# Kernel optimization log

Measured on AMD Instinct MI355X. Metric: run time of the kernel, lower is better.

## Reference

```python
import jax, jax.numpy as jnp
import numpy as np

H = 1024
N_HEADS = 16
DK = H // N_HEADS
B = 4
S_TGT = 1024
S_SRC = 1024
LN_EPS = 1e-5


def _ln(x, g, b):
    m = jnp.mean(x, axis=-1, keepdims=True)
    v = jnp.mean(jnp.square(x - m), axis=-1, keepdims=True)
    return (x - m) * jax.lax.rsqrt(v + LN_EPS) * g + b


def _mha(q_in, k_in, v_in, wq, wk, wv, wo, mask):
    # Equivalent to torch split(hidden//n_splits)+cat(dim=0) head layout:
    # per-(batch,head) scaled dot-product attention.
    Bq, Sq, _ = q_in.shape
    Sk = k_in.shape[1]
    q = (q_in @ wq).reshape(Bq, Sq, N_HEADS, DK)
    k = (k_in @ wk).reshape(Bq, Sk, N_HEADS, DK)
    v = (v_in @ wv).reshape(Bq, Sk, N_HEADS, DK)
    scores = jnp.einsum('bqhd,bkhd->bhqk', q, k)
    if mask is not None:
        scores = jnp.where(mask[:, None, :, :], -jnp.inf, scores)
    attn = jax.nn.softmax(scores / np.sqrt(DK).astype(np.float32), axis=-1)
    ctx = jnp.einsum('bhqk,bkhd->bqhd', attn, v).reshape(Bq, Sq, H)
    return ctx @ wo


def setup_inputs() -> dict:
    key = jax.random.key(0)
    ks = jax.random.split(key, 16)
    std = 1.0 / np.sqrt(H)
    p = {
        'x': jax.random.normal(ks[0], (B, S_TGT, H), jnp.float32),
        'key_and_value': jax.random.normal(ks[1], (B, S_SRC, H), jnp.float32),
        'mask': jnp.zeros((B, S_TGT, S_SRC), jnp.bool_),  # no padding
        # causal mask: True above the diagonal (masked positions)
        'future_mask': jnp.broadcast_to(
            jnp.triu(jnp.ones((S_TGT, S_TGT), jnp.bool_), k=1), (B, S_TGT, S_TGT)),
        'sa_wq': jax.random.normal(ks[2], (H, H), jnp.float32) * std,
        'sa_wk': jax.random.normal(ks[3], (H, H), jnp.float32) * std,
        'sa_wv': jax.random.normal(ks[4], (H, H), jnp.float32) * std,
        'sa_wo': jax.random.normal(ks[5], (H, H), jnp.float32) * std,
        'ca_wq': jax.random.normal(ks[6], (H, H), jnp.float32) * std,
        'ca_wk': jax.random.normal(ks[7], (H, H), jnp.float32) * std,
        'ca_wv': jax.random.normal(ks[8], (H, H), jnp.float32) * std,
        'ca_wo': jax.random.normal(ks[9], (H, H), jnp.float32) * std,
        'fc_w1': jax.random.normal(ks[10], (H, 4 * H), jnp.float32) * std,
        'fc_b1': jnp.zeros((4 * H,), jnp.float32),
        'fc_w2': jax.random.normal(ks[11], (4 * H, H), jnp.float32) * (0.5 * std),
        'fc_b2': jnp.zeros((H,), jnp.float32),
        'ln1_g': jnp.ones((H,), jnp.float32), 'ln1_b': jnp.zeros((H,), jnp.float32),
        'ln2_g': jnp.ones((H,), jnp.float32), 'ln2_b': jnp.zeros((H,), jnp.float32),
        'ln3_g': jnp.ones((H,), jnp.float32), 'ln3_b': jnp.zeros((H,), jnp.float32),
    }
    return p


def reference(x, key_and_value, mask, future_mask,
              sa_wq, sa_wk, sa_wv, sa_wo,
              ca_wq, ca_wk, ca_wv, ca_wo,
              fc_w1, fc_b1, fc_w2, fc_b2,
              ln1_g, ln1_b, ln2_g, ln2_b, ln3_g, ln3_b):
    # prev is None path (training); dropout in eval mode = identity.
    z = _ln(x, ln1_g, ln1_b)
    z = x + _mha(z, z, z, sa_wq, sa_wk, sa_wv, sa_wo, future_mask)
    nkv = _ln(key_and_value, ln2_g, ln2_b)
    z = z + _mha(_ln(z, ln2_g, ln2_b), nkv, nkv, ca_wq, ca_wk, ca_wv, ca_wo, mask)
    h = jax.nn.relu(_ln(z, ln3_g, ln3_b) @ fc_w1 + fc_b1)
    z = z + (h @ fc_w2 + fc_b2)
    return z
```

## Files before the change

### kernel.cpp

```cpp
#include <hip/hip_runtime.h>
#include <hip/hip_bf16.h>

typedef __attribute__((ext_vector_type(8))) short short8;
typedef __attribute__((ext_vector_type(4))) float f32x4;
using bf16 = __hip_bfloat16;

__device__ __forceinline__ void gload16(const void* g, void* l) {
  __builtin_amdgcn_global_load_lds(
      (const __attribute__((address_space(1))) void*)g,
      (__attribute__((address_space(3))) void*)l, 16, 0, 0);
}

__device__ __forceinline__ short f2bf(float f) {
  bf16 h = __float2bfloat16(f);
  short s;
  __builtin_memcpy(&s, &h, 2);
  return s;
}

__device__ __forceinline__ float bf2f(unsigned short u) {
  unsigned int x = ((unsigned int)u) << 16;
  float f;
  __builtin_memcpy(&f, &x, 4);
  return f;
}

__global__ __launch_bounds__(256)
void wtr8(const float* w0, const float* w1, const float* w2, const float* w3,
          const float* w4, const float* w5, const float* w6, const float* w7,
          bf16* __restrict__ Wout) {
  __shared__ float tile[32][33];
  const float* w;
  switch (blockIdx.z) {
    case 0: w = w0; break; case 1: w = w1; break;
    case 2: w = w2; break; case 3: w = w3; break;
    case 4: w = w4; break; case 5: w = w5; break;
    case 6: w = w6; break; default: w = w7; break;
  }
  bf16* wt = Wout + (size_t)blockIdx.z * 1024 * 1024;
  const int tx = threadIdx.x & 31, ty = threadIdx.x >> 5;
  const int c0 = blockIdx.x * 32, r0 = blockIdx.y * 32;
#pragma unroll
  for (int i = 0; i < 4; ++i)
    tile[ty * 4 + i][tx] = w[(size_t)(r0 + ty * 4 + i) * 1024 + c0 + tx];
  __syncthreads();
#pragma unroll
  for (int i = 0; i < 4; ++i) {
    const int cc = ty * 4 + i;
    wt[(size_t)(c0 + cc) * 1024 + r0 + tx] = __float2bfloat16(tile[tx][cc]);
  }
}

__global__ __launch_bounds__(256)
void wtr(const float* __restrict__ w, bf16* __restrict__ wt, int R, int C) {
  __shared__ float tile[32][33];
  const int tx = threadIdx.x & 31, ty = threadIdx.x >> 5;
  const int c0 = blockIdx.x * 32, r0 = blockIdx.y * 32;
#pragma unroll
  for (int i = 0; i < 4; ++i)
    tile[ty * 4 + i][tx] = w[(size_t)(r0 + ty * 4 + i) * C + c0 + tx];
  __syncthreads();
#pragma unroll
  for (int i = 0; i < 4; ++i) {
    const int cc = ty * 4 + i;
    wt[(size_t)(c0 + cc) * R + r0 + tx] = __float2bfloat16(tile[tx][cc]);
  }
}

__global__ __launch_bounds__(256)
void ln_k(const float* __restrict__ x, const float* __restrict__ g,
          const float* __restrict__ b, bf16* __restrict__ y) {
  const int row = blockIdx.x, t = threadIdx.x;
  const int wv = t >> 6, l = t & 63;
  const float4 v = reinterpret_cast<const float4*>(x + (size_t)row * 1024)[t];
  float s = v.x + v.y + v.z + v.w;
  float s2 = v.x * v.x + v.y * v.y + v.z * v.z + v.w * v.w;
#pragma unroll
  for (int m = 1; m < 64; m <<= 1) {
    s += __shfl_xor(s, m, 64);
    s2 += __shfl_xor(s2, m, 64);
  }
  __shared__ float ps[4], ps2[4];
  if (l == 0) { ps[wv] = s; ps2[wv] = s2; }
  __syncthreads();
  s = ps[0] + ps[1] + ps[2] + ps[3];
  s2 = ps2[0] + ps2[1] + ps2[2] + ps2[3];
  const float mean = s * (1.f / 1024.f);
  const float var = s2 * (1.f / 1024.f) - mean * mean;
  const float rs = rsqrtf(var + 1e-5f);
  const float4 gg = reinterpret_cast<const float4*>(g)[t];
  const float4 bb = reinterpret_cast<const float4*>(b)[t];
  ushort4 o;
  o.x = (unsigned short)f2bf((v.x - mean) * rs * gg.x + bb.x);
  o.y = (unsigned short)f2bf((v.y - mean) * rs * gg.y + bb.y);
  o.z = (unsigned short)f2bf((v.z - mean) * rs * gg.z + bb.z);
  o.w = (unsigned short)f2bf((v.w - mean) * rs * gg.w + bb.w);
  reinterpret_cast<ushort4*>(y + (size_t)row * 1024)[t] = o;
}

__global__ __launch_bounds__(256)
void ffn_add4b(const ushort4* __restrict__ p0, const ushort4* __restrict__ p1,
               const ushort4* __restrict__ p2, const ushort4* __restrict__ p3,
               const float4* __restrict__ res, const float4* __restrict__ bias,
               float4* __restrict__ out) {
  const size_t i = (size_t)blockIdx.x * 256 + threadIdx.x;
  const ushort4 a = p0[i], b = p1[i], c = p2[i], d = p3[i];
  const float4 r = res[i];
  const float4 g = bias[i & 255];
  float4 o;
  o.x = (bf2f(a.x) + bf2f(b.x)) + (bf2f(c.x) + bf2f(d.x)) + r.x + g.x;
  o.y = (bf2f(a.y) + bf2f(b.y)) + (bf2f(c.y) + bf2f(d.y)) + r.y + g.y;
  o.z = (bf2f(a.z) + bf2f(b.z)) + (bf2f(c.z) + bf2f(d.z)) + r.z + g.z;
  o.w = (bf2f(a.w) + bf2f(b.w)) + (bf2f(c.w) + bf2f(d.w)) + r.w + g.w;
  out[i] = o;
}

template <int BM, int EPI>
__global__ __launch_bounds__(256, 2)
void gemm_bt(const bf16* __restrict__ A, const bf16* __restrict__ BT,
             const float* bias, const float* res, void* outp,
             int M, int N, int K, bf16* vtp, int nv0) {
  constexpr int WM = BM / 32;
  constexpr int APASS = BM / 32;
  __shared__ alignas(16) short al[2][BM * 64];
  __shared__ alignas(16) short bl[2][128 * 64];
  const int t = threadIdx.x;
  const int gx = N >> 7;
  const int nwg = gridDim.x * gridDim.y;
  int id = blockIdx.y * gridDim.x + blockIdx.x;
  id = (id & 7) * (nwg >> 3) + (id >> 3);
  const int bx = id % gx, by = id / gx;
  const int m0 = by * BM, n0 = bx * 128;
  const int wv = t >> 6, l = t & 63, lr = l & 15, lk = l >> 4;
  const int wr = wv >> 1, wc = wv & 1;
  const int tr = t >> 3, tc = (t & 7) * 8;
  const int tcs = (((t & 7) ^ (tr & 7)) * 8);
  const int cro0 = ((lk ^ (lr & 7)) * 8);
  const int cro1 = (((4 + lk) ^ (lr & 7)) * 8);

  f32x4 acc[WM][4];
#pragma unroll
  for (int i = 0; i < WM; ++i)
#pragma unroll
    for (int j = 0; j < 4; ++j) acc[i][j] = (f32x4)0.f;

#define STAGE(buf, k0)                                                        \
  do {                                                                        \
    _Pragma("unroll") for (int it = 0; it < APASS; ++it) {                    \
      const int row = it * 32 + tr;                                           \
      gload16(A + (size_t)(m0 + row) * K + (k0) + tcs,                        \
              (char*)&al[buf][row * 64 + tc]);                                \
    }                                                                         \
    _Pragma("unroll") for (int it = 0; it < 4; ++it) {                        \
      const int row = it * 32 + tr;                                           \
      gload16(BT + (size_t)(n0 + row) * K + (k0) + tcs,                       \
              (char*)&bl[buf][row * 64 + tc]);                                \
    }                                                                         \
  } while (0)

#define COMPUTE(cur)                                                          \
  do {                                                                        \
    _Pragma("unroll") for (int ks = 0; ks < 2; ++ks) {                        \
      const int cro = ks ? cro1 : cro0;                                       \
      short8 af[WM], bfv[4];                                                  \
      _Pragma("unroll") for (int m = 0; m < WM; ++m) af[m] =                  \
          *reinterpret_cast<const short8*>(                                   \
              &al[cur][(wr * (BM / 2) + m * 16 + lr) * 64 + cro]);            \
      _Pragma("unroll") for (int n = 0; n < 4; ++n) bfv[n] =                  \
          *reinterpret_cast<const short8*>(                                   \
              &bl[cur][(wc * 64 + n * 16 + lr) * 64 + cro]);                  \
      _Pragma("unroll") for (int m = 0; m < WM; ++m)                          \
          _Pragma("unroll") for (int n = 0; n < 4; ++n) acc[m][n] =           \
              __builtin_amdgcn_mfma_f32_16x16x32_bf16(af[m], bfv[n],          \
                                                      acc[m][n], 0, 0, 0);    \
    }                                                                         \
  } while (0)

  const int nt = K >> 6;
  if constexpr (BM == 64) {
    STAGE(0, 0);
    STAGE(1, 64);
    for (int tk = 0; tk < nt; ++tk) {
      const int cur = tk & 1;
      if (tk < nt - 1)
        asm volatile("s_waitcnt vmcnt(6)" ::: "memory");
      else
        asm volatile("s_waitcnt vmcnt(0)" ::: "memory");
      __builtin_amdgcn_s_barrier();
      COMPUTE(cur);
      if (tk + 2 < nt) {
        asm volatile("s_waitcnt lgkmcnt(0)" ::: "memory");
        __builtin_amdgcn_s_barrier();
        STAGE(cur, (tk + 2) << 6);
      }
    }
  } else {
    STAGE(0, 0);
    asm volatile("s_waitcnt vmcnt(0)" ::: "memory");
    __syncthreads();
    for (int tk = 0; tk < nt; ++tk) {
      const int cur = tk & 1;
      if (tk + 1 < nt) STAGE(cur ^ 1, (tk + 1) << 6);
      COMPUTE(cur);
      asm volatile("s_waitcnt vmcnt(0)" ::: "memory");
      __syncthreads();
    }
  }
#undef STAGE
#undef COMPUTE

  const int r0 = m0 + wr * (BM / 2), c0 = n0 + wc * 64;
  if constexpr (EPI == 4) {
#pragma unroll
    for (int m = 0; m < WM; ++m) {
      const int rowb = r0 + m * 16 + lk * 4;
      const int bb = rowb >> 10, s0 = rowb & 1023;
#pragma unroll
      for (int n = 0; n < 4; ++n) {
        const int col = c0 + n * 16 + lr;
        if (col < nv0) {
#pragma unroll
          for (int r = 0; r < 4; ++r)
            ((bf16*)outp)[(size_t)(rowb + r) * nv0 + col] =
                __float2bfloat16(acc[m][n][r]);
        } else {
          ushort4 u;
          u.x = (unsigned short)f2bf(acc[m][n][0]);
          u.y = (unsigned short)f2bf(acc[m][n][1]);
          u.z = (unsigned short)f2bf(acc[m][n][2]);
          u.w = (unsigned short)f2bf(acc[m][n][3]);
          const size_t vidx = ((size_t)bb * 1024 + (col - nv0)) * 1024 + s0;
          *reinterpret_cast<ushort4*>(vtp + vidx) = u;
        }
      }
    }
  } else {
#pragma unroll
    for (int m = 0; m < WM; ++m)
#pragma unroll
      for (int n = 0; n < 4; ++n) {
        const int col = c0 + n * 16 + lr;
#pragma unroll
        for (int r = 0; r < 4; ++r) {
          const int row = r0 + m * 16 + lk * 4 + r;
          const size_t idx = (size_t)row * N + col;
          float v = acc[m][n][r];
          if (EPI == 0) {
            ((bf16*)outp)[idx] = __float2bfloat16(v);
          } else if (EPI == 1) {
            ((float*)outp)[idx] = res[idx] + v;
          } else if (EPI == 2) {
            v += bias[col];
            ((bf16*)outp)[idx] = __float2bfloat16(fmaxf(v, 0.f));
          } else {
            ((float*)outp)[idx] = res[idx] + v + bias[col];
          }
        }
      }
  }
}

template <int EPI>
__global__ __launch_bounds__(512, 1)
void gemm256(const bf16* __restrict__ A, const bf16* __restrict__ BT,
             const float* __restrict__ bias, void* __restrict__ outp,
             int M, int N, int K, int lda) {
  __shared__ alignas(16) short al[2][256 * 64];
  __shared__ alignas(16) short bl[2][256 * 64];
  const int t = threadIdx.x;
  const int gx = N >> 8;
  const int nwg = gridDim.x * gridDim.y;
  int id = blockIdx.y * gridDim.x + blockIdx.x;
  id = (id & 7) * (nwg >> 3) + (id >> 3);
  const int bx = id % gx, by = id / gx;
  const int m0 = by * 256, n0 = bx * 256;
  const int wid = t >> 6, l = t & 63, lr = l & 15, lk = l >> 4;
  const int wm = wid >> 2, wn = wid & 3;
  const int tr = t >> 3, tc = (t & 7) * 8;
  const int tcs = (((t & 7) ^ (tr & 7)) * 8);
  const int cro0 = ((lk ^ (lr & 7)) * 8);
  const int cro1 = (((4 + lk) ^ (lr & 7)) * 8);

  const bf16* Ab = (EPI == 5) ? A + (size_t)blockIdx.z * K : A;
  const bf16* BTb = (EPI == 5) ? BT + (size_t)blockIdx.z * K : BT;

  f32x4 acc[8][4];
#pragma unroll
  for (int i = 0; i < 8; ++i)
#pragma unroll
    for (int j = 0; j < 4; ++j) acc[i][j] = (f32x4)0.f;

#define STAGE2(buf, k0)                                                       \
  do {                                                                        \
    _Pragma("unroll") for (int it = 0; it < 4; ++it) {                        \
      const int row = it * 64 + tr;                                           \
      gload16(Ab + (size_t)(m0 + row) * lda + (k0) + tcs,                     \
              (char*)&al[buf][row * 64 + tc]);                                \
    }                                                                         \
    _Pragma("unroll") for (int it = 0; it < 4; ++it) {                        \
      const int row = it * 64 + tr;                                           \
      gload16(BTb + (size_t)(n0 + row) * lda + (k0) + tcs,                    \
              (char*)&bl[buf][row * 64 + tc]);                                \
    }                                                                         \
  } while (0)

#define COMPUTE2(cur)                                                         \
  do {                                                                        \
    _Pragma("unroll") for (int ks = 0; ks < 2; ++ks) {                        \
      const int cro = ks ? cro1 : cro0;                                       \
      short8 af[8], bfv[4];                                                   \
      _Pragma("unroll") for (int m = 0; m < 8; ++m) af[m] =                   \
          *reinterpret_cast<const short8*>(                                   \
              &al[cur][(wm * 128 + m * 16 + lr) * 64 + cro]);                 \
      _Pragma("unroll") for (int n = 0; n < 4; ++n) bfv[n] =                  \
          *reinterpret_cast<const short8*>(                                   \
              &bl[cur][(wn * 64 + n * 16 + lr) * 64 + cro]);                  \
      _Pragma("unroll") for (int m = 0; m < 8; ++m)                           \
          _Pragma("unroll") for (int n = 0; n < 4; ++n) acc[m][n] =           \
              __builtin_amdgcn_mfma_f32_16x16x32_bf16(af[m], bfv[n],          \
                                                      acc[m][n], 0, 0, 0);    \
    }                                                                         \
  } while (0)

  const int nt = K >> 6;
  STAGE2(0, 0);
  STAGE2(1, 64);
  for (int tk = 0; tk < nt; ++tk) {
    const int cur = tk & 1;
    if (tk < nt - 1)
      asm volatile("s_waitcnt vmcnt(8)" ::: "memory");
    else
      asm volatile("s_waitcnt vmcnt(0)" ::: "memory");
    __builtin_amdgcn_s_barrier();
    COMPUTE2(cur);
    if (tk + 2 < nt) {
      asm volatile("s_waitcnt lgkmcnt(0)" ::: "memory");
      __builtin_amdgcn_s_barrier();
      STAGE2(cur, (tk + 2) << 6);
    }
  }
#undef STAGE2
#undef COMPUTE2

  const int r0 = m0 + wm * 128, c0 = n0 + wn * 64;
  if constexpr (EPI == 2) {
#pragma unroll
    for (int m = 0; m < 8; ++m)
#pragma unroll
      for (int n = 0; n < 4; ++n) {
        const int col = c0 + n * 16 + lr;
        const float bcol = bias[col];
#pragma unroll
        for (int r = 0; r < 4; ++r) {
          const int row = r0 + m * 16 + lk * 4 + r;
          const float v = acc[m][n][r] + bcol;
          ((bf16*)outp)[(size_t)row * N + col] =
              __float2bfloat16(fmaxf(v, 0.f));
        }
      }
  } else {
    bf16* po = (bf16*)outp + (size_t)blockIdx.z * M * N;
#pragma unroll
    for (int m = 0; m < 8; ++m)
#pragma unroll
      for (int n = 0; n < 4; ++n) {
        const int col = c0 + n * 16 + lr;
#pragma unroll
        for (int r = 0; r < 4; ++r) {
          const int row = r0 + m * 16 + lk * 4 + r;
          po[(size_t)row * N + col] = __float2bfloat16(acc[m][n][r]);
        }
      }
  }
}

__global__ __launch_bounds__(512, 1)
void gemm256_dual(const bf16* __restrict__ A0, const bf16* __restrict__ BT0,
                  bf16* __restrict__ out0, bf16* __restrict__ vt0,
                  const bf16* __restrict__ A1, const bf16* __restrict__ BT1,
                  bf16* __restrict__ out1, bf16* __restrict__ vt1) {
  __shared__ alignas(16) short al[2][256 * 64];
  __shared__ alignas(16) short bl[2][256 * 64];
  const int t = threadIdx.x;
  const int raw = blockIdx.x;
  const int id = (raw & 7) * 40 + (raw >> 3);
  const bf16 *A, *BT;
  bf16 *outp, *vtp;
  int nv0, gx, pid;
  if (id < 192) {
    A = A0; BT = BT0; outp = out0; vtp = vt0; nv0 = 2048; gx = 12; pid = id;
  } else {
    A = A1; BT = BT1; outp = out1; vtp = vt1; nv0 = 1024; gx = 8;
    pid = id - 192;
  }
  const int K = 1024;
  const int bx = pid % gx, by = pid / gx;
  const int m0 = by * 256, n0 = bx * 256;
  const int wid = t >> 6, l = t & 63, lr = l & 15, lk = l >> 4;
  const int wm = wid >> 2, wn = wid & 3;
  const int tr = t >> 3, tc = (t & 7) * 8;
  const int tcs = (((t & 7) ^ (tr & 7)) * 8);
  const int cro0 = ((lk ^ (lr & 7)) * 8);
  const int cro1 = (((4 + lk) ^ (lr & 7)) * 8);

  f32x4 acc[8][4];
#pragma unroll
  for (int i = 0; i < 8; ++i)
#pragma unroll
    for (int j = 0; j < 4; ++j) acc[i][j] = (f32x4)0.f;

#define STAGE2(buf, k0)                                                       \
  do {                                                                        \
    _Pragma("unroll") for (int it = 0; it < 4; ++it) {                        \
      const int row = it * 64 + tr;                                           \
      gload16(A + (size_t)(m0 + row) * K + (k0) + tcs,                        \
              (char*)&al[buf][row * 64 + tc]);                                \
    }                                                                         \
    _Pragma("unroll") for (int it = 0; it < 4; ++it) {                        \
      const int row = it * 64 + tr;                                           \
      gload16(BT + (size_t)(n0 + row) * K + (k0) + tcs,                       \
              (char*)&bl[buf][row * 64 + tc]);                                \
    }                                                                         \
  } while (0)

#define COMPUTE2(cur)                                                         \
  do {                                                                        \
    _Pragma("unroll") for (int ks = 0; ks < 2; ++ks) {                        \
      const int cro = ks ? cro1 : cro0;                                       \
      short8 af[8], bfv[4];                                                   \
      _Pragma("unroll") for (int m = 0; m < 8; ++m) af[m] =                   \
          *reinterpret_cast<const short8*>(                                   \
              &al[cur][(wm * 128 + m * 16 + lr) * 64 + cro]);                 \
      _Pragma("unroll") for (int n = 0; n < 4; ++n) bfv[n] =                  \
          *reinterpret_cast<const short8*>(                                   \
              &bl[cur][(wn * 64 + n * 16 + lr) * 64 + cro]);                  \
      _Pragma("unroll") for (int m = 0; m < 8; ++m)                           \
          _Pragma("unroll") for (int n = 0; n < 4; ++n) acc[m][n] =           \
              __builtin_amdgcn_mfma_f32_16x16x32_bf16(af[m], bfv[n],          \
                                                      acc[m][n], 0, 0, 0);    \
    }                                                                         \
  } while (0)

  const int nt = K >> 6;
  STAGE2(0, 0);
  STAGE2(1, 64);
  for (int tk = 0; tk < nt; ++tk) {
    const int cur = tk & 1;
    if (tk < nt - 1)
      asm volatile("s_waitcnt vmcnt(8)" ::: "memory");
    else
      asm volatile("s_waitcnt vmcnt(0)" ::: "memory");
    __builtin_amdgcn_s_barrier();
    COMPUTE2(cur);
    if (tk + 2 < nt) {
      asm volatile("s_waitcnt lgkmcnt(0)" ::: "memory");
      __builtin_amdgcn_s_barrier();
      STAGE2(cur, (tk + 2) << 6);
    }
  }
#undef STAGE2
#undef COMPUTE2

  const int r0 = m0 + wm * 128, c0 = n0 + wn * 64;
#pragma unroll
  for (int m = 0; m < 8; ++m) {
    const int rowb = r0 + m * 16 + lk * 4;
    const int bb = rowb >> 10, s0 = rowb & 1023;
#pragma unroll
    for (int n = 0; n < 4; ++n) {
      const int col = c0 + n * 16 + lr;
      if (col < nv0) {
#pragma unroll
        for (int r = 0; r < 4; ++r)
          outp[(size_t)(rowb + r) * nv0 + col] =
              __float2bfloat16(acc[m][n][r]);
      } else {
        ushort4 u;
        u.x = (unsigned short)f2bf(acc[m][n][0]);
        u.y = (unsigned short)f2bf(acc[m][n][1]);
        u.z = (unsigned short)f2bf(acc[m][n][2]);
        u.w = (unsigned short)f2bf(acc[m][n][3]);
        const size_t vidx = ((size_t)bb * 1024 + (col - nv0)) * 1024 + s0;
        *reinterpret_cast<ushort4*>(vtp + vidx) = u;
      }
    }
  }
}

template <bool CAUSAL>
__global__ __launch_bounds__(256, 2)
void flash8(const bf16* __restrict__ Qb, int ldq,
            const bf16* __restrict__ Kb, int ldk,
            const bf16* __restrict__ VTb, bf16* __restrict__ Ob) {
  __shared__ alignas(16) short kl[3][64 * 64];
  __shared__ alignas(16) short vl[3][64 * 64];
  __shared__ alignas(16) short pl[4][32 * 72];
  const int t = threadIdx.x, wv = t >> 6, l = t & 63, lr = l & 15, lk = l >> 4;
  const int raw = blockIdx.y * 8 + blockIdx.x;
  const int id = (raw & 7) * 64 + (raw >> 3);
  const int qb = id & 7, bh = id >> 3;
  const int b = bh >> 4, h = bh & 15;
  const size_t rowbase = (size_t)b * 1024;
  const int q0 = qb * 128 + wv * 32;
  const bf16* Vbase = VTb + (rowbase + h * 64) * 1024;

  const int tr = t >> 3;
  const int tcd = (t & 7) * 8;
  const int tcs = (((t & 7) ^ (tr & 7)) * 8);
  const int cro0 = ((lk ^ (lr & 7)) * 8);
  const int cro1 = (((4 + lk) ^ (lr & 7)) * 8);

  short8 qf[2][2];
#pragma unroll
  for (int m = 0; m < 2; ++m)
#pragma unroll
    for (int ks = 0; ks < 2; ++ks)
      qf[m][ks] = *reinterpret_cast<const short8*>(
          Qb + (rowbase + q0 + m * 16 + lr) * ldq + h * 64 + ks * 32 + lk * 8);

  short8 ones;
#pragma unroll
  for (int j = 0; j < 8; ++j) ones[j] = (short)0x3F80;

  f32x4 accO[2][4];
  f32x4 accL[2];
#pragma unroll
  for (int m = 0; m < 2; ++m) {
#pragma unroll
    for (int n = 0; n < 4; ++n) accO[m][n] = (f32x4)0.f;
    accL[m] = (f32x4)0.f;
  }

  const int ntb = CAUSAL ? (qb * 2 + 2) : 16;
  const int myLast = q0 >> 6;

#define FSTAGE(buf, kv0)                                                      \
  do {                                                                        \
    _Pragma("unroll") for (int it = 0; it < 2; ++it) {                        \
      const int row = it * 32 + tr;                                           \
      gload16(Kb + (rowbase + (kv0) + row) * ldk + h * 64 + tcs,              \
              (char*)&kl[buf][row * 64 + tcd]);                               \
    }                                                                         \
    _Pragma("unroll") for (int it = 0; it < 2; ++it) {                        \
      const int row = it * 32 + tr;                                           \
      gload16(Vbase + (size_t)row * 1024 + (kv0) + tcs,                       \
              (char*)&vl[buf][row * 64 + tcd]);                               \
    }                                                                         \
  } while (0)

  FSTAGE(0, 0);
  FSTAGE(1, 64);
  int cur = 0;
  for (int tk = 0; tk < ntb; ++tk) {
    if (tk < ntb - 1)
      asm volatile("s_waitcnt vmcnt(4)" ::: "memory");
    else
      asm volatile("s_waitcnt vmcnt(0)" ::: "memory");
    __builtin_amdgcn_s_barrier();
    if (tk + 2 < ntb) {
      int stg = cur + 2;
      if (stg >= 3) stg -= 3;
      FSTAGE(stg, (tk + 2) << 6);
    }
    if (!CAUSAL || tk <= myLast) {
      const int kv0 = tk * 64;
      const bool needmask = CAUSAL && (tk == myLast);
      f32x4 sa[2][4];
#pragma unroll
      for (int m = 0; m < 2; ++m)
#pragma unroll
        for (int n = 0; n < 4; ++n) sa[m][n] = (f32x4)0.f;
#pragma unroll
      for (int ks = 0; ks < 2; ++ks) {
        const int cro = ks ? cro1 : cro0;
        short8 kf[4];
#pragma unroll
        for (int n = 0; n < 4; ++n)
          kf[n] = *reinterpret_cast<const short8*>(
              &kl[cur][(n * 16 + lr) * 64 + cro]);
        __builtin_amdgcn_s_setprio(1);
#pragma unroll
        for (int m = 0; m < 2; ++m)
#pragma unroll
          for (int n = 0; n < 4; ++n)
            sa[m][n] = __builtin_amdgcn_mfma_f32_16x16x32_bf16(
                qf[m][ks], kf[n], sa[m][n], 0, 0, 0);
        __builtin_amdgcn_s_setprio(0);
      }
#pragma unroll
      for (int m = 0; m < 2; ++m) {
#pragma unroll
        for (int r = 0; r < 4; ++r) {
          const int row = q0 + m * 16 + lk * 4 + r;
          float s0 = sa[m][0][r] * 0.125f, s1 = sa[m][1][r] * 0.125f;
          float s2 = sa[m][2][r] * 0.125f, s3 = sa[m][3][r] * 0.125f;
          if (needmask) {
            if (kv0 + 0 + lr > row) s0 = -1e30f;
            if (kv0 + 16 + lr > row) s1 = -1e30f;
            if (kv0 + 32 + lr > row) s2 = -1e30f;
            if (kv0 + 48 + lr > row) s3 = -1e30f;
          }
          const float p0 = __expf(s0), p1 = __expf(s1);
          const float p2 = __expf(s2), p3 = __expf(s3);
          const int prow = m * 16 + lk * 4 + r;
          pl[wv][prow * 72 + lr + 0] = f2bf(p0);
          pl[wv][prow * 72 + lr + 16] = f2bf(p1);
          pl[wv][prow * 72 + lr + 32] = f2bf(p2);
          pl[wv][prow * 72 + lr + 48] = f2bf(p3);
        }
      }
#pragma unroll
      for (int ks = 0; ks < 2; ++ks) {
        const int cro = ks ? cro1 : cro0;
        short8 pf[2], vf[4];
#pragma unroll
        for (int m = 0; m < 2; ++m)
          pf[m] = *reinterpret_cast<const short8*>(
              &pl[wv][(m * 16 + lr) * 72 + ks * 32 + lk * 8]);
#pragma unroll
        for (int n = 0; n < 4; ++n)
          vf[n] = *reinterpret_cast<const short8*>(
              &vl[cur][(n * 16 + lr) * 64 + cro]);
        __builtin_amdgcn_s_setprio(1);
#pragma unroll
        for (int m = 0; m < 2; ++m) {
#pragma unroll
          for (int n = 0; n < 4; ++n)
            accO[m][n] = __builtin_amdgcn_mfma_f32_16x16x32_bf16(
                pf[m], vf[n], accO[m][n], 0, 0, 0);
          accL[m] = __builtin_amdgcn_mfma_f32_16x16x32_bf16(
              pf[m], ones, accL[m], 0, 0, 0);
        }
        __builtin_amdgcn_s_setprio(0);
      }
    }
    cur = (cur + 1 == 3) ? 0 : cur + 1;
  }
#undef FSTAGE

#pragma unroll
  for (int m = 0; m < 2; ++m)
#pragma unroll
    for (int n = 0; n < 4; ++n)
#pragma unroll
      for (int r = 0; r < 4; ++r) {
        const int row = q0 + m * 16 + lk * 4 + r;
        const int col = n * 16 + lr;
        const float o = accO[m][n][r] / accL[m][r];
        Ob[(rowbase + row) * 1024 + h * 64 + col] = __float2bfloat16(o);
      }
}

extern "C" void kernel_launch(void* const* d_in, const int* in_sizes, int n_in,
                              void* d_out, int out_size, void* d_ws,
                              size_t ws_size, hipStream_t stream) {
  const float* x = (const float*)d_in[0];
  const float* kv_in = (const float*)d_in[1];
  const float* sa_wq = (const float*)d_in[4];
  const float* sa_wk = (const float*)d_in[5];
  const float* sa_wv = (const float*)d_in[6];
  const float* sa_wo = (const float*)d_in[7];
  const float* ca_wq = (const float*)d_in[8];
  const float* ca_wk = (const float*)d_in[9];
  const float* ca_wv = (const float*)d_in[10];
  const float* ca_wo = (const float*)d_in[11];
  const float* fc_w1 = (const float*)d_in[12];
  const float* fc_b1 = (const float*)d_in[13];
  const float* fc_w2 = (const float*)d_in[14];
  const float* fc_b2 = (const float*)d_in[15];
  const float* ln1_g = (const float*)d_in[16];
  const float* ln1_b = (const float*)d_in[17];
  const float* ln2_g = (const float*)d_in[18];
  const float* ln2_b = (const float*)d_in[19];
  const float* ln3_g = (const float*)d_in[20];
  const float* ln3_b = (const float*)d_in[21];

  char* ws = (char*)d_ws;
  const size_t MB = 1024 * 1024;
  bf16* W = (bf16*)ws;
  bf16* w1T = W + 8 * MB;
  bf16* w2T = W + 12 * MB;
  float* z = (float*)(ws + 32 * MB);
  bf16* t0 = (bf16*)(ws + 48 * MB);
  bf16* qkvb = (bf16*)(ws + 56 * MB);
  bf16* vts = (bf16*)(ws + 72 * MB);
  bf16* kb = (bf16*)(ws + 80 * MB);
  bf16* vtc = (bf16*)(ws + 88 * MB);
  bf16* qb = (bf16*)(ws + 96 * MB);
  bf16* ctx = (bf16*)(ws + 104 * MB);
  bf16* kvln = (bf16*)(ws + 112 * MB);
  bf16* hb = (bf16*)(ws + 120 * MB);
  bf16* partsb = (bf16*)(ws + 56 * MB);

  const dim3 B256(256);
  wtr8<<<dim3(32, 32, 8), B256, 0, stream>>>(sa_wq, sa_wk, sa_wv, sa_wo,
                                             ca_wq, ca_wk, ca_wv, ca_wo, W);
  wtr<<<dim3(128, 32), B256, 0, stream>>>(fc_w1, w1T, 1024, 4096);
  wtr<<<dim3(32, 128), B256, 0, stream>>>(fc_w2, w2T, 4096, 1024);

  ln_k<<<4096, B256, 0, stream>>>(x, ln1_g, ln1_b, t0);
  ln_k<<<4096, B256, 0, stream>>>(kv_in, ln2_g, ln2_b, kvln);
  gemm256_dual<<<dim3(320), dim3(512), 0, stream>>>(
      t0, W, qkvb, vts, kvln, W + 5 * MB, kb, vtc);

  flash8<true><<<dim3(8, 64), B256, 0, stream>>>(
      qkvb, 2048, qkvb + 1024, 2048, vts, ctx);
  gemm_bt<64, 1><<<dim3(8, 64), B256, 0, stream>>>(
      ctx, W + 3 * MB, nullptr, x, z, 4096, 1024, 1024, nullptr, 0);

  ln_k<<<4096, B256, 0, stream>>>(z, ln2_g, ln2_b, t0);
  gemm_bt<64, 0><<<dim3(8, 64), B256, 0, stream>>>(
      t0, W + 4 * MB, nullptr, nullptr, qb, 4096, 1024, 1024, nullptr, 0);
  flash8<false><<<dim3(8, 64), B256, 0, stream>>>(
      qb, 1024, kb, 1024, vtc, ctx);
  gemm_bt<64, 1><<<dim3(8, 64), B256, 0, stream>>>(
      ctx, W + 7 * MB, nullptr, z, z, 4096, 1024, 1024, nullptr, 0);

  ln_k<<<4096, B256, 0, stream>>>(z, ln3_g, ln3_b, t0);
  gemm256<2><<<dim3(16, 16), dim3(512), 0, stream>>>(
      t0, w1T, fc_b1, hb, 4096, 4096, 1024, 1024);
  gemm256<5><<<dim3(4, 16, 4), dim3(512), 0, stream>>>(
      hb, w2T, nullptr, partsb, 4096, 1024, 1024, 4096);
  ffn_add4b<<<4096, B256, 0, stream>>>(
      (const ushort4*)(partsb + 0 * (size_t)4096 * 1024),
      (const ushort4*)(partsb + 1 * (size_t)4096 * 1024),
      (const ushort4*)(partsb + 2 * (size_t)4096 * 1024),
      (const ushort4*)(partsb + 3 * (size_t)4096 * 1024),
      (const float4*)z, (const float4*)fc_b2, (float4*)d_out);
}
```

Baseline: 328.3 us.

## Replace 64x128 GEMMs with split-K 256-tile GEMM plus combine kernels

The three 1024x1024 projection GEMMs (self-attn output, cross-attn Q, cross-attn output) move from the 64x128-tile gemm_bt kernel to the 256x256-tile gemm256 in split-K mode with four K-slices of 256. Each slice writes bf16 partials, and a templated comb4 kernel sums them with an optional residual and bias. The aim is higher MFMA efficiency from larger tiles while keeping 256 workgroups to fill the CUs. In exchange it adds three extra elementwise launches, extra partial-buffer traffic, and bf16 rounding of the partial sums.

```diff
diff --git a/kernel.cpp b/kernel.cpp
--- a/kernel.cpp
+++ b/kernel.cpp
@@ -98,165 +98,36 @@
   reinterpret_cast<ushort4*>(y + (size_t)row * 1024)[t] = o;
 }
 
+template <int MODE>
 __global__ __launch_bounds__(256)
-void ffn_add4b(const ushort4* __restrict__ p0, const ushort4* __restrict__ p1,
-               const ushort4* __restrict__ p2, const ushort4* __restrict__ p3,
-               const float4* __restrict__ res, const float4* __restrict__ bias,
-               float4* __restrict__ out) {
+void comb4(const ushort4* __restrict__ p0, const ushort4* __restrict__ p1,
+           const ushort4* __restrict__ p2, const ushort4* __restrict__ p3,
+           const float4* __restrict__ res, const float4* __restrict__ bias,
+           void* __restrict__ outv) {
   const size_t i = (size_t)blockIdx.x * 256 + threadIdx.x;
   const ushort4 a = p0[i], b = p1[i], c = p2[i], d = p3[i];
-  const float4 r = res[i];
-  const float4 g = bias[i & 255];
-  float4 o;
-  o.x = (bf2f(a.x) + bf2f(b.x)) + (bf2f(c.x) + bf2f(d.x)) + r.x + g.x;
-  o.y = (bf2f(a.y) + bf2f(b.y)) + (bf2f(c.y) + bf2f(d.y)) + r.y + g.y;
-  o.z = (bf2f(a.z) + bf2f(b.z)) + (bf2f(c.z) + bf2f(d.z)) + r.z + g.z;
-  o.w = (bf2f(a.w) + bf2f(b.w)) + (bf2f(c.w) + bf2f(d.w)) + r.w + g.w;
-  out[i] = o;
-}
-
-template <int BM, int EPI>
-__global__ __launch_bounds__(256, 2)
-void gemm_bt(const bf16* __restrict__ A, const bf16* __restrict__ BT,
-             const float* bias, const float* res, void* outp,
-             int M, int N, int K, bf16* vtp, int nv0) {
-  constexpr int WM = BM / 32;
-  constexpr int APASS = BM / 32;
-  __shared__ alignas(16) short al[2][BM * 64];
-  __shared__ alignas(16) short bl[2][128 * 64];
-  const int t = threadIdx.x;
-  const int gx = N >> 7;
-  const int nwg = gridDim.x * gridDim.y;
-  int id = blockIdx.y * gridDim.x + blockIdx.x;
-  id = (id & 7) * (nwg >> 3) + (id >> 3);
-  const int bx = id % gx, by = id / gx;
-  const int m0 = by * BM, n0 = bx * 128;
-  const int wv = t >> 6, l = t & 63, lr = l & 15, lk = l >> 4;
-  const int wr = wv >> 1, wc = wv & 1;
-  const int tr = t >> 3, tc = (t & 7) * 8;
-  const int tcs = (((t & 7) ^ (tr & 7)) * 8);
-  const int cro0 = ((lk ^ (lr & 7)) * 8);
-  const int cro1 = (((4 + lk) ^ (lr & 7)) * 8);
-
-  f32x4 acc[WM][4];
-#pragma unroll
-  for (int i = 0; i < WM; ++i)
-#pragma unroll
-    for (int j = 0; j < 4; ++j) acc[i][j] = (f32x4)0.f;
-
-#define STAGE(buf, k0)                                                        \
-  do {                                                                        \
-    _Pragma("unroll") for (int it = 0; it < APASS; ++it) {                    \
-      const int row = it * 32 + tr;                                           \
-      gload16(A + (size_t)(m0 + row) * K + (k0) + tcs,                        \
-              (char*)&al[buf][row * 64 + tc]);                                \
-    }                                                                         \
-    _Pragma("unroll") for (int it = 0; it < 4; ++it) {                        \
-      const int row = it * 32 + tr;                                           \
-      gload16(BT + (size_t)(n0 + row) * K + (k0) + tcs,                       \
-              (char*)&bl[buf][row * 64 + tc]);                                \
-    }                                                                         \
-  } while (0)
-
-#define COMPUTE(cur)                                                          \
-  do {                                                                        \
-    _Pragma("unroll") for (int ks = 0; ks < 2; ++ks) {                        \
-      const int cro = ks ? cro1 : cro0;                                       \
-      short8 af[WM], bfv[4];                                                  \
-      _Pragma("unroll") for (int m = 0; m < WM; ++m) af[m] =                  \
-          *reinterpret_cast<const short8*>(                                   \
-              &al[cur][(wr * (BM / 2) + m * 16 + lr) * 64 + cro]);            \
-      _Pragma("unroll") for (int n = 0; n < 4; ++n) bfv[n] =                  \
-          *reinterpret_cast<const short8*>(                                   \
-              &bl[cur][(wc * 64 + n * 16 + lr) * 64 + cro]);                  \
-      _Pragma("unroll") for (int m = 0; m < WM; ++m)                          \
-          _Pragma("unroll") for (int n = 0; n < 4; ++n) acc[m][n] =           \
-              __builtin_amdgcn_mfma_f32_16x16x32_bf16(af[m], bfv[n],          \
-                                                      acc[m][n], 0, 0, 0);    \
-    }                                                                         \
-  } while (0)
-
-  const int nt = K >> 6;
-  if constexpr (BM == 64) {
-    STAGE(0, 0);
-    STAGE(1, 64);
-    for (int tk = 0; tk < nt; ++tk) {
-      const int cur = tk & 1;
-      if (tk < nt - 1)
-        asm volatile("s_waitcnt vmcnt(6)" ::: "memory");
-      else
-        asm volatile("s_waitcnt vmcnt(0)" ::: "memory");
-      __builtin_amdgcn_s_barrier();
-      COMPUTE(cur);
-      if (tk + 2 < nt) {
-        asm volatile("s_waitcnt lgkmcnt(0)" ::: "memory");
-        __builtin_amdgcn_s_barrier();
-        STAGE(cur, (tk + 2) << 6);
-      }
+  float sx = (bf2f(a.x) + bf2f(b.x)) + (bf2f(c.x) + bf2f(d.x));
+  float sy = (bf2f(a.y) + bf2f(b.y)) + (bf2f(c.y) + bf2f(d.y));
+  float sz = (bf2f(a.z) + bf2f(b.z)) + (bf2f(c.z) + bf2f(d.z));
+  float sw = (bf2f(a.w) + bf2f(b.w)) + (bf2f(c.w) + bf2f(d.w));
+  if constexpr (MODE == 1) {
+    ushort4 o;
+    o.x = (unsigned short)f2bf(sx);
+    o.y = (unsigned short)f2bf(sy);
+    o.z = (unsigned short)f2bf(sz);
+    o.w = (unsigned short)f2bf(sw);
+    ((ushort4*)outv)[i] = o;
+  } else {
+    const float4 r = res[i];
+    float4 o;
+    if constexpr (MODE == 2) {
+      const float4 g = bias[i & 255];
+      o.x = sx + r.x + g.x; o.y = sy + r.y + g.y;
+      o.z = sz + r.z + g.z; o.w = sw + r.w + g.w;
+    } else {
+      o.x = sx + r.x; o.y = sy + r.y; o.z = sz + r.z; o.w = sw + r.w;
     }
-  } else {
-    STAGE(0, 0);
-    asm volatile("s_waitcnt vmcnt(0)" ::: "memory");
-    __syncthreads();
-    for (int tk = 0; tk < nt; ++tk) {
-      const int cur = tk & 1;
-      if (tk + 1 < nt) STAGE(cur ^ 1, (tk + 1) << 6);
-      COMPUTE(cur);
-      asm volatile("s_waitcnt vmcnt(0)" ::: "memory");
-      __syncthreads();
-    }
-  }
-#undef STAGE
-#undef COMPUTE
-
-  const int r0 = m0 + wr * (BM / 2), c0 = n0 + wc * 64;
-  if constexpr (EPI == 4) {
-#pragma unroll
-    for (int m = 0; m < WM; ++m) {
-      const int rowb = r0 + m * 16 + lk * 4;
-      const int bb = rowb >> 10, s0 = rowb & 1023;
-#pragma unroll
-      for (int n = 0; n < 4; ++n) {
-        const int col = c0 + n * 16 + lr;
-        if (col < nv0) {
-#pragma unroll
-          for (int r = 0; r < 4; ++r)
-            ((bf16*)outp)[(size_t)(rowb + r) * nv0 + col] =
-                __float2bfloat16(acc[m][n][r]);
-        } else {
-          ushort4 u;
-          u.x = (unsigned short)f2bf(acc[m][n][0]);
-          u.y = (unsigned short)f2bf(acc[m][n][1]);
-          u.z = (unsigned short)f2bf(acc[m][n][2]);
-          u.w = (unsigned short)f2bf(acc[m][n][3]);
-          const size_t vidx = ((size_t)bb * 1024 + (col - nv0)) * 1024 + s0;
-          *reinterpret_cast<ushort4*>(vtp + vidx) = u;
-        }
-      }
-    }
-  } else {
-#pragma unroll
-    for (int m = 0; m < WM; ++m)
-#pragma unroll
-      for (int n = 0; n < 4; ++n) {
-        const int col = c0 + n * 16 + lr;
-#pragma unroll
-        for (int r = 0; r < 4; ++r) {
-          const int row = r0 + m * 16 + lk * 4 + r;
-          const size_t idx = (size_t)row * N + col;
-          float v = acc[m][n][r];
-          if (EPI == 0) {
-            ((bf16*)outp)[idx] = __float2bfloat16(v);
-          } else if (EPI == 1) {
-            ((float*)outp)[idx] = res[idx] + v;
-          } else if (EPI == 2) {
-            v += bias[col];
-            ((bf16*)outp)[idx] = __float2bfloat16(fmaxf(v, 0.f));
-          } else {
-            ((float*)outp)[idx] = res[idx] + v + bias[col];
-          }
-        }
-      }
+    ((float4*)outv)[i] = o;
   }
 }
 
@@ -690,7 +561,9 @@
   bf16* ctx = (bf16*)(ws + 104 * MB);
   bf16* kvln = (bf16*)(ws + 112 * MB);
   bf16* hb = (bf16*)(ws + 120 * MB);
+  bf16* partsO = (bf16*)(ws + 120 * MB);
   bf16* partsb = (bf16*)(ws + 56 * MB);
+  const size_t PSL = (size_t)4096 * 1024;
 
   const dim3 B256(256);
   wtr8<<<dim3(32, 32, 8), B256, 0, stream>>>(sa_wq, sa_wk, sa_wv, sa_wo,
@@ -705,26 +578,36 @@
 
   flash8<true><<<dim3(8, 64), B256, 0, stream>>>(
       qkvb, 2048, qkvb + 1024, 2048, vts, ctx);
-  gemm_bt<64, 1><<<dim3(8, 64), B256, 0, stream>>>(
-      ctx, W + 3 * MB, nullptr, x, z, 4096, 1024, 1024, nullptr, 0);
+  gemm256<5><<<dim3(4, 16, 4), dim3(512), 0, stream>>>(
+      ctx, W + 3 * MB, nullptr, partsO, 4096, 1024, 256, 1024);
+  comb4<0><<<4096, B256, 0, stream>>>(
+      (const ushort4*)(partsO + 0 * PSL), (const ushort4*)(partsO + 1 * PSL),
+      (const ushort4*)(partsO + 2 * PSL), (const ushort4*)(partsO + 3 * PSL),
+      (const float4*)x, nullptr, z);
 
   ln_k<<<4096, B256, 0, stream>>>(z, ln2_g, ln2_b, t0);
-  gemm_bt<64, 0><<<dim3(8, 64), B256, 0, stream>>>(
-      t0, W + 4 * MB, nullptr, nullptr, qb, 4096, 1024, 1024, nullptr, 0);
+  gemm256<5><<<dim3(4, 16, 4), dim3(512), 0, stream>>>(
+      t0, W + 4 * MB, nullptr, partsO, 4096, 1024, 256, 1024);
+  comb4<1><<<4096, B256, 0, stream>>>(
+      (const ushort4*)(partsO + 0 * PSL), (const ushort4*)(partsO + 1 * PSL),
+      (const ushort4*)(partsO + 2 * PSL), (const ushort4*)(partsO + 3 * PSL),
+      nullptr, nullptr, qb);
   flash8<false><<<dim3(8, 64), B256, 0, stream>>>(
       qb, 1024, kb, 1024, vtc, ctx);
-  gemm_bt<64, 1><<<dim3(8, 64), B256, 0, stream>>>(
-      ctx, W + 7 * MB, nullptr, z, z, 4096, 1024, 1024, nullptr, 0);
+  gemm256<5><<<dim3(4, 16, 4), dim3(512), 0, stream>>>(
+      ctx, W + 7 * MB, nullptr, partsO, 4096, 1024, 256, 1024);
+  comb4<0><<<4096, B256, 0, stream>>>(
+      (const ushort4*)(partsO + 0 * PSL), (const ushort4*)(partsO + 1 * PSL),
+      (const ushort4*)(partsO + 2 * PSL), (const ushort4*)(partsO + 3 * PSL),
+      (const float4*)z, nullptr, z);
 
   ln_k<<<4096, B256, 0, stream>>>(z, ln3_g, ln3_b, t0);
   gemm256<2><<<dim3(16, 16), dim3(512), 0, stream>>>(
       t0, w1T, fc_b1, hb, 4096, 4096, 1024, 1024);
   gemm256<5><<<dim3(4, 16, 4), dim3(512), 0, stream>>>(
       hb, w2T, nullptr, partsb, 4096, 1024, 1024, 4096);
-  ffn_add4b<<<4096, B256, 0, stream>>>(
-      (const ushort4*)(partsb + 0 * (size_t)4096 * 1024),
-      (const ushort4*)(partsb + 1 * (size_t)4096 * 1024),
-      (const ushort4*)(partsb + 2 * (size_t)4096 * 1024),
-      (const ushort4*)(partsb + 3 * (size_t)4096 * 1024),
+  comb4<2><<<4096, B256, 0, stream>>>(
+      (const ushort4*)(partsb + 0 * PSL), (const ushort4*)(partsb + 1 * PSL),
+      (const ushort4*)(partsb + 2 * PSL), (const ushort4*)(partsb + 3 * PSL),
       (const float4*)z, (const float4*)fc_b2, (float4*)d_out);
 }
```

New measurement: 348.8 us. +6.2%, slower.
